# Optimization experiments

Measured on AMD Instinct MI355X. Metric: run time of the kernel, lower is better.

The kernel has to match this reference:

```python
import jax, jax.numpy as jnp
import numpy as np

B, T, K = 256, 512, 128
LR_MULT = 1.0  # learning_rate_multiplier


def setup_inputs() -> dict:
    key = jax.random.key(0)
    k1, k2, k3 = jax.random.split(key, 3)
    emissions = jax.random.normal(k1, (B, T, K), dtype=jnp.float32)
    mask = jax.random.randint(k2, (B, T), 0, 2, dtype=jnp.int32)
    # learned CRF transition matrix (stand-in for Orthogonal init)
    transition_weight = jax.random.normal(k3, (K, K), dtype=jnp.float32)
    return {"emissions": emissions, "mask": mask, "transition_weight": transition_weight}


def reference(emissions, mask, transition_weight):
    # Viterbi decode (tfa.text.crf_decode semantics): sequence_lengths = sum(mask),
    # state frozen for steps t >= length, output tags multiplied by mask.
    mask = mask.astype(jnp.int32)
    lengths = jnp.sum(mask, axis=1)                       # [B]
    trans = transition_weight * LR_MULT                   # [K,K]
    Tn = emissions.shape[1]

    init_state = emissions[:, 0, :]                       # [B,K] viterbi scores at t=0
    ts = jnp.arange(1, Tn)                                # steps 1..T-1
    em_rest = jnp.swapaxes(emissions[:, 1:, :], 0, 1)     # [T-1,B,K]

    def fwd_step(state, inp):
        e_t, t = inp                                      # e_t: [B,K]
        scores = state[:, :, None] + trans[None, :, :]    # [B, K_prev, K_cur]
        bp = jnp.argmax(scores, axis=1).astype(jnp.int32)  # [B,K] best prev tag
        new_state = jnp.max(scores, axis=1) + e_t         # [B,K]
        valid = (t < lengths)[:, None]                    # step valid iff t <= len-1
        return jnp.where(valid, new_state, state), bp

    last_state, bps = jax.lax.scan(fwd_step, init_state, (em_rest, ts))  # bps: [T-1,B,K]
    last_tag = jnp.argmax(last_state, axis=1).astype(jnp.int32)  # tag at pos length-1

    def bwd_step(tag, inp):
        bp_t, t = inp                                     # bp_t: [B,K]
        prev = jnp.take_along_axis(bp_t, tag[:, None], axis=1)[:, 0]
        tag = jnp.where(t < lengths, prev, tag)           # carry tag beyond seq end
        return tag, tag

    # reverse scan: ys[i] = tag at position i, for positions 0..T-2
    _, tags_prefix = jax.lax.scan(bwd_step, last_tag, (bps, ts), reverse=True)
    tags = jnp.concatenate([jnp.swapaxes(tags_prefix, 0, 1), last_tag[:, None]], axis=1)
    return tags * mask
```

## Files before the change

### kernel.cpp

```cpp
#include <hip/hip_runtime.h>

#define NB 256
#define NT 512
#define NK 128

__device__ __forceinline__ void upd(float v, int i, float& bv, int& bi) {
    bool g = v > bv;
    bv = g ? v : bv;
    bi = g ? i : bi;
}

__global__ __launch_bounds__(256, 1)
void crf_decode_kernel(const float* __restrict__ em,
                       const int* __restrict__ mask,
                       const float* __restrict__ trans,
                       int* __restrict__ out) {
    __shared__ alignas(16) float state_sh[NK];
    __shared__ float part_val[256];
    __shared__ int   part_idx[256];
    __shared__ unsigned char bp_sh[(NT - 1) * NK];
    __shared__ int tags_sh[NT];
    __shared__ int len_sh;
    __shared__ int lt_sh;

    const int b    = blockIdx.x;
    const int tid  = threadIdx.x;
    const int j    = tid & (NK - 1);
    const int half = tid >> 7;
    const long base = (long)b * NT * NK;

    int s = mask[b * NT + tid] + mask[b * NT + tid + 256];
    #pragma unroll
    for (int off = 32; off > 0; off >>= 1) s += __shfl_down(s, off, 64);
    if (tid == 0) len_sh = 0;
    __syncthreads();
    if ((tid & 63) == 0) atomicAdd(&len_sh, s);

    if (half == 0) state_sh[j] = em[base + j];

    float treg[64];
    #pragma unroll
    for (int ii = 0; ii < 64; ++ii)
        treg[ii] = trans[(half * 64 + ii) * NK + j];

    __syncthreads();
    const int len = len_sh;

    for (int t = 1; t < len; ++t) {
        float e = 0.0f;
        if (half == 0) e = em[base + t * NK + j];

        float bv0 = -3.4e38f, bv1 = -3.4e38f, bv2 = -3.4e38f, bv3 = -3.4e38f;
        int   bi0 = 0, bi1 = 1, bi2 = 2, bi3 = 3;
        const float4* sp = (const float4*)&state_sh[half * 64];
        #pragma unroll
        for (int g = 0; g < 16; ++g) {
            float4 sv = sp[g];
            const int ib = half * 64 + g * 4;
            upd(sv.x + treg[g * 4 + 0], ib + 0, bv0, bi0);
            upd(sv.y + treg[g * 4 + 1], ib + 1, bv1, bi1);
            upd(sv.z + treg[g * 4 + 2], ib + 2, bv2, bi2);
            upd(sv.w + treg[g * 4 + 3], ib + 3, bv3, bi3);
        }
        bool tk;
        tk = (bv1 > bv0) || (bv1 == bv0 && bi1 < bi0);
        float mv0 = tk ? bv1 : bv0; int mi0 = tk ? bi1 : bi0;
        tk = (bv3 > bv2) || (bv3 == bv2 && bi3 < bi2);
        float mv1 = tk ? bv3 : bv2; int mi1 = tk ? bi3 : bi2;
        tk = (mv1 > mv0) || (mv1 == mv0 && mi1 < mi0);
        float bv = tk ? mv1 : mv0;  int bi = tk ? mi1 : mi0;

        part_val[tid] = bv;
        part_idx[tid] = bi;
        __syncthreads();
        if (half == 0) {
            float ov = part_val[tid + 128];
            int   oi = part_idx[tid + 128];
            bool take = ov > bv;
            float nv = (take ? ov : bv) + e;
            int   ni = take ? oi : bi;
            state_sh[j] = nv;
            bp_sh[(t - 1) * NK + j] = (unsigned char)ni;
        }
        __syncthreads();
    }

    if (tid < 64) {
        float v0 = state_sh[tid], v1 = state_sh[tid + 64];
        bool take = v1 > v0;
        float v = take ? v1 : v0;
        int  ix = take ? tid + 64 : tid;
        #pragma unroll
        for (int off = 32; off > 0; off >>= 1) {
            float vo = __shfl_xor(v, off, 64);
            int   io = __shfl_xor(ix, off, 64);
            bool t2 = (vo > v) || (vo == v && io < ix);
            v  = t2 ? vo : v;
            ix = t2 ? io : ix;
        }
        if (tid == 0) lt_sh = ix;
    }
    __syncthreads();
    const int last_tag = lt_sh;
    const int lm1 = (len > 0) ? (len - 1) : 0;

    for (int p = tid; p < NT; p += 256)
        if (p >= lm1) tags_sh[p] = last_tag;
    __syncthreads();

    if (tid == 0) {
        int tag = last_tag;
        for (int p = lm1 - 1; p >= 0; --p) {
            tag = (int)bp_sh[p * NK + tag];
            tags_sh[p] = tag;
        }
    }
    __syncthreads();

    for (int p = tid; p < NT; p += 256) {
        int mv = mask[b * NT + p];
        out[b * NT + p] = mv ? tags_sh[p] : 0;
    }
}

extern "C" void kernel_launch(void* const* d_in, const int* in_sizes, int n_in,
                              void* d_out, int out_size, void* d_ws, size_t ws_size,
                              hipStream_t stream) {
    const float* em    = (const float*)d_in[0];
    const int*   mask  = (const int*)d_in[1];
    const float* trans = (const float*)d_in[2];
    int* out = (int*)d_out;
    hipLaunchKernelGGL(crf_decode_kernel, dim3(NB), dim3(256), 0, stream,
                       em, mask, trans, out);
}
```

Baseline: 411.2 us.

## Use one thread per tag with double-buffered state and prefetched emissions

Shrinks the block from 256 to 128 threads so each thread reduces over all 128 previous tags itself. This removes the cross-half partial-result exchange, and double-buffering the state array leaves one barrier per time step instead of two. Emissions are prefetched from global memory eight steps ahead into a double-buffered shared array, taking the global load off the per-step critical path. In exchange, each step's serial max/argmax chain is twice as long on fewer waves, and each thread keeps 128 transition values in registers.

```diff
diff --git a/kernel.cpp b/kernel.cpp
--- a/kernel.cpp
+++ b/kernel.cpp
@@ -3,6 +3,7 @@
 #define NB 256
 #define NT 512
 #define NK 128
+#define GRP 8
 
 __device__ __forceinline__ void upd(float v, int i, float& bv, int& bi) {
     bool g = v > bv;
@@ -10,86 +11,86 @@
     bi = g ? i : bi;
 }
 
-__global__ __launch_bounds__(256, 1)
+__global__ __launch_bounds__(128, 1)
 void crf_decode_kernel(const float* __restrict__ em,
                        const int* __restrict__ mask,
                        const float* __restrict__ trans,
                        int* __restrict__ out) {
-    __shared__ alignas(16) float state_sh[NK];
-    __shared__ float part_val[256];
-    __shared__ int   part_idx[256];
+    __shared__ alignas(16) float state_sh[2][NK];
+    __shared__ float e_sh[2][GRP][NK];
     __shared__ unsigned char bp_sh[(NT - 1) * NK];
     __shared__ int tags_sh[NT];
-    __shared__ int len_sh;
-    __shared__ int lt_sh;
+    __shared__ float red_v[2];
+    __shared__ int   red_i[2];
+    __shared__ int len_sh, lt_sh;
 
-    const int b    = blockIdx.x;
-    const int tid  = threadIdx.x;
-    const int j    = tid & (NK - 1);
-    const int half = tid >> 7;
+    const int b = blockIdx.x;
+    const int j = threadIdx.x;
     const long base = (long)b * NT * NK;
 
-    int s = mask[b * NT + tid] + mask[b * NT + tid + 256];
+    float ld[GRP];
+    #pragma unroll
+    for (int k = 0; k < GRP; ++k) ld[k] = em[base + (1 + k) * NK + j];
+
+    int s = 0;
+    #pragma unroll
+    for (int k = 0; k < 4; ++k) s += mask[b * NT + j + 128 * k];
     #pragma unroll
     for (int off = 32; off > 0; off >>= 1) s += __shfl_down(s, off, 64);
-    if (tid == 0) len_sh = 0;
+    if (j == 0) len_sh = 0;
     __syncthreads();
-    if ((tid & 63) == 0) atomicAdd(&len_sh, s);
+    if ((j & 63) == 0) atomicAdd(&len_sh, s);
 
-    if (half == 0) state_sh[j] = em[base + j];
+    float treg[NK];
+    #pragma unroll
+    for (int i = 0; i < NK; ++i) treg[i] = trans[i * NK + j];
 
-    float treg[64];
-    #pragma unroll
-    for (int ii = 0; ii < 64; ++ii)
-        treg[ii] = trans[(half * 64 + ii) * NK + j];
-
+    state_sh[0][j] = em[base + j];
     __syncthreads();
     const int len = len_sh;
 
-    for (int t = 1; t < len; ++t) {
-        float e = 0.0f;
-        if (half == 0) e = em[base + t * NK + j];
+    int cur = 0, cb = 0;
+    for (int t0 = 1; t0 < len; t0 += GRP) {
+        #pragma unroll
+        for (int k = 0; k < GRP; ++k) e_sh[cb][k][j] = ld[k];
+        #pragma unroll
+        for (int k = 0; k < GRP; ++k) {
+            int tt = t0 + GRP + k; tt = tt < NT ? tt : NT - 1;
+            ld[k] = em[base + tt * NK + j];
+        }
+        const int te = (t0 + GRP < len) ? t0 + GRP : len;
+        for (int t = t0; t < te; ++t) {
+            const float4* sp = (const float4*)state_sh[cur];
+            float bv0 = -3.4e38f, bv1 = -3.4e38f, bv2 = -3.4e38f, bv3 = -3.4e38f;
+            int   bi0 = 0, bi1 = 1, bi2 = 2, bi3 = 3;
+            #pragma unroll
+            for (int g = 0; g < 32; ++g) {
+                float4 sv = sp[g];
+                upd(sv.x + treg[4 * g + 0], 4 * g + 0, bv0, bi0);
+                upd(sv.y + treg[4 * g + 1], 4 * g + 1, bv1, bi1);
+                upd(sv.z + treg[4 * g + 2], 4 * g + 2, bv2, bi2);
+                upd(sv.w + treg[4 * g + 3], 4 * g + 3, bv3, bi3);
+            }
+            bool tk;
+            tk = (bv1 > bv0) || (bv1 == bv0 && bi1 < bi0);
+            float mv0 = tk ? bv1 : bv0; int mi0 = tk ? bi1 : bi0;
+            tk = (bv3 > bv2) || (bv3 == bv2 && bi3 < bi2);
+            float mv1 = tk ? bv3 : bv2; int mi1 = tk ? bi3 : bi2;
+            tk = (mv1 > mv0) || (mv1 == mv0 && mi1 < mi0);
+            float bv = tk ? mv1 : mv0;  int bi = tk ? mi1 : mi0;
 
-        float bv0 = -3.4e38f, bv1 = -3.4e38f, bv2 = -3.4e38f, bv3 = -3.4e38f;
-        int   bi0 = 0, bi1 = 1, bi2 = 2, bi3 = 3;
-        const float4* sp = (const float4*)&state_sh[half * 64];
-        #pragma unroll
-        for (int g = 0; g < 16; ++g) {
-            float4 sv = sp[g];
-            const int ib = half * 64 + g * 4;
-            upd(sv.x + treg[g * 4 + 0], ib + 0, bv0, bi0);
-            upd(sv.y + treg[g * 4 + 1], ib + 1, bv1, bi1);
-            upd(sv.z + treg[g * 4 + 2], ib + 2, bv2, bi2);
-            upd(sv.w + treg[g * 4 + 3], ib + 3, bv3, bi3);
+            float e = e_sh[cb][t - t0][j];
+            state_sh[cur ^ 1][j] = bv + e;
+            bp_sh[(t - 1) * NK + j] = (unsigned char)bi;
+            __syncthreads();
+            cur ^= 1;
         }
-        bool tk;
-        tk = (bv1 > bv0) || (bv1 == bv0 && bi1 < bi0);
-        float mv0 = tk ? bv1 : bv0; int mi0 = tk ? bi1 : bi0;
-        tk = (bv3 > bv2) || (bv3 == bv2 && bi3 < bi2);
-        float mv1 = tk ? bv3 : bv2; int mi1 = tk ? bi3 : bi2;
-        tk = (mv1 > mv0) || (mv1 == mv0 && mi1 < mi0);
-        float bv = tk ? mv1 : mv0;  int bi = tk ? mi1 : mi0;
-
-        part_val[tid] = bv;
-        part_idx[tid] = bi;
-        __syncthreads();
-        if (half == 0) {
-            float ov = part_val[tid + 128];
-            int   oi = part_idx[tid + 128];
-            bool take = ov > bv;
-            float nv = (take ? ov : bv) + e;
-            int   ni = take ? oi : bi;
-            state_sh[j] = nv;
-            bp_sh[(t - 1) * NK + j] = (unsigned char)ni;
-        }
-        __syncthreads();
+        cb ^= 1;
     }
 
-    if (tid < 64) {
-        float v0 = state_sh[tid], v1 = state_sh[tid + 64];
-        bool take = v1 > v0;
-        float v = take ? v1 : v0;
-        int  ix = take ? tid + 64 : tid;
+    {
+        float v = state_sh[cur][j];
+        int  ix = j;
         #pragma unroll
         for (int off = 32; off > 0; off >>= 1) {
             float vo = __shfl_xor(v, off, 64);
@@ -98,17 +99,24 @@
             v  = t2 ? vo : v;
             ix = t2 ? io : ix;
         }
-        if (tid == 0) lt_sh = ix;
+        if ((j & 63) == 0) { red_v[j >> 6] = v; red_i[j >> 6] = ix; }
+        __syncthreads();
+        if (j == 0) {
+            float v0 = red_v[0], v1 = red_v[1];
+            int   i0 = red_i[0], i1 = red_i[1];
+            bool t2 = (v1 > v0) || (v1 == v0 && i1 < i0);
+            lt_sh = t2 ? i1 : i0;
+        }
     }
     __syncthreads();
     const int last_tag = lt_sh;
     const int lm1 = (len > 0) ? (len - 1) : 0;
 
-    for (int p = tid; p < NT; p += 256)
+    for (int p = j; p < NT; p += 128)
         if (p >= lm1) tags_sh[p] = last_tag;
     __syncthreads();
 
-    if (tid == 0) {
+    if (j == 0) {
         int tag = last_tag;
         for (int p = lm1 - 1; p >= 0; --p) {
             tag = (int)bp_sh[p * NK + tag];
@@ -117,7 +125,7 @@
     }
     __syncthreads();
 
-    for (int p = tid; p < NT; p += 256) {
+    for (int p = j; p < NT; p += 128) {
         int mv = mask[b * NT + p];
         out[b * NT + p] = mv ? tags_sh[p] : 0;
     }
@@ -130,6 +138,6 @@
     const int*   mask  = (const int*)d_in[1];
     const float* trans = (const float*)d_in[2];
     int* out = (int*)d_out;
-    hipLaunchKernelGGL(crf_decode_kernel, dim3(NB), dim3(256), 0, stream,
+    hipLaunchKernelGGL(crf_decode_kernel, dim3(NB), dim3(128), 0, stream,
                        em, mask, trans, out);
 }
```

New measurement: 679.0 us. 65.1% more time.

## Pair halves within a wavefront, double-buffer state, prefetch emissions in groups

Applied to the files above, without the earlier changes.

Remaps threads so the two halves of each tag's reduction sit in the same wavefront, replacing the shared-memory partial exchange with a cross-lane shuffle. State is double-buffered so each time step needs one barrier instead of two. Emission values are prefetched eight steps ahead into registers to hide global load latency in the serial recurrence. This raises register pressure through the extra prefetch registers, and the tail loop loads emissions without prefetching.

```diff
diff --git a/kernel.cpp b/kernel.cpp
--- a/kernel.cpp
+++ b/kernel.cpp
@@ -3,6 +3,7 @@
 #define NB 256
 #define NT 512
 #define NK 128
+#define GRP 8
 
 __device__ __forceinline__ void upd(float v, int i, float& bv, int& bi) {
     bool g = v > bv;
@@ -15,18 +16,17 @@
                        const int* __restrict__ mask,
                        const float* __restrict__ trans,
                        int* __restrict__ out) {
-    __shared__ alignas(16) float state_sh[NK];
-    __shared__ float part_val[256];
-    __shared__ int   part_idx[256];
+    __shared__ alignas(16) float state_sh[2][NK];
     __shared__ unsigned char bp_sh[(NT - 1) * NK];
     __shared__ int tags_sh[NT];
-    __shared__ int len_sh;
-    __shared__ int lt_sh;
+    __shared__ int len_sh, lt_sh;
 
     const int b    = blockIdx.x;
     const int tid  = threadIdx.x;
-    const int j    = tid & (NK - 1);
-    const int half = tid >> 7;
+    const int l    = tid & 63;
+    const int w    = tid >> 6;
+    const int jj   = (w << 5) | (l & 31);
+    const int half = l >> 5;
     const long base = (long)b * NT * NK;
 
     int s = mask[b * NT + tid] + mask[b * NT + tid + 256];
@@ -34,33 +34,39 @@
     for (int off = 32; off > 0; off >>= 1) s += __shfl_down(s, off, 64);
     if (tid == 0) len_sh = 0;
     __syncthreads();
-    if ((tid & 63) == 0) atomicAdd(&len_sh, s);
-
-    if (half == 0) state_sh[j] = em[base + j];
+    if (l == 0) atomicAdd(&len_sh, s);
 
     float treg[64];
     #pragma unroll
     for (int ii = 0; ii < 64; ++ii)
-        treg[ii] = trans[(half * 64 + ii) * NK + j];
+        treg[ii] = trans[(half * 64 + ii) * NK + jj];
 
+    if (half == 0) state_sh[0][jj] = em[base + jj];
     __syncthreads();
     const int len = len_sh;
 
-    for (int t = 1; t < len; ++t) {
-        float e = 0.0f;
-        if (half == 0) e = em[base + t * NK + j];
+    int cur = 0;
+    int t = 1;
 
+    float ld[GRP];
+    #pragma unroll
+    for (int k = 0; k < GRP; ++k) {
+        int tt = t + k; tt = tt < NT ? tt : NT - 1;
+        ld[k] = em[base + tt * NK + jj];
+    }
+
+    auto step = [&](int tt, float e) {
+        const float4* sp = (const float4*)&state_sh[cur][half * 64];
         float bv0 = -3.4e38f, bv1 = -3.4e38f, bv2 = -3.4e38f, bv3 = -3.4e38f;
-        int   bi0 = 0, bi1 = 1, bi2 = 2, bi3 = 3;
-        const float4* sp = (const float4*)&state_sh[half * 64];
+        int bi0 = half*64 + 0, bi1 = half*64 + 1, bi2 = half*64 + 2, bi3 = half*64 + 3;
         #pragma unroll
         for (int g = 0; g < 16; ++g) {
             float4 sv = sp[g];
-            const int ib = half * 64 + g * 4;
-            upd(sv.x + treg[g * 4 + 0], ib + 0, bv0, bi0);
-            upd(sv.y + treg[g * 4 + 1], ib + 1, bv1, bi1);
-            upd(sv.z + treg[g * 4 + 2], ib + 2, bv2, bi2);
-            upd(sv.w + treg[g * 4 + 3], ib + 3, bv3, bi3);
+            const int ib = half * 64 + 4 * g;
+            upd(sv.x + treg[4*g + 0], ib + 0, bv0, bi0);
+            upd(sv.y + treg[4*g + 1], ib + 1, bv1, bi1);
+            upd(sv.z + treg[4*g + 2], ib + 2, bv2, bi2);
+            upd(sv.w + treg[4*g + 3], ib + 3, bv3, bi3);
         }
         bool tk;
         tk = (bv1 > bv0) || (bv1 == bv0 && bi1 < bi0);
@@ -70,23 +76,38 @@
         tk = (mv1 > mv0) || (mv1 == mv0 && mi1 < mi0);
         float bv = tk ? mv1 : mv0;  int bi = tk ? mi1 : mi0;
 
-        part_val[tid] = bv;
-        part_idx[tid] = bi;
+        float vo = __shfl_xor(bv, 32, 64);
+        int   io = __shfl_xor(bi, 32, 64);
+        bool t2 = (vo > bv) || (vo == bv && io < bi);
+        float fv = t2 ? vo : bv;
+        int   fi = t2 ? io : bi;
+
+        if (half == 0) state_sh[cur ^ 1][jj] = fv + e;
+        else           bp_sh[(tt - 1) * NK + jj] = (unsigned char)fi;
         __syncthreads();
-        if (half == 0) {
-            float ov = part_val[tid + 128];
-            int   oi = part_idx[tid + 128];
-            bool take = ov > bv;
-            float nv = (take ? ov : bv) + e;
-            int   ni = take ? oi : bi;
-            state_sh[j] = nv;
-            bp_sh[(t - 1) * NK + j] = (unsigned char)ni;
+        cur ^= 1;
+    };
+
+    while (t + GRP <= len) {
+        float ec[GRP];
+        #pragma unroll
+        for (int k = 0; k < GRP; ++k) ec[k] = ld[k];
+        #pragma unroll
+        for (int k = 0; k < GRP; ++k) {
+            int tt = t + GRP + k; tt = tt < NT ? tt : NT - 1;
+            ld[k] = em[base + tt * NK + jj];
         }
-        __syncthreads();
+        #pragma unroll
+        for (int k = 0; k < GRP; ++k) step(t + k, ec[k]);
+        t += GRP;
+    }
+    for (; t < len; ++t) {
+        float e = em[base + t * NK + jj];
+        step(t, e);
     }
 
     if (tid < 64) {
-        float v0 = state_sh[tid], v1 = state_sh[tid + 64];
+        float v0 = state_sh[cur][tid], v1 = state_sh[cur][tid + 64];
         bool take = v1 > v0;
         float v = take ? v1 : v0;
         int  ix = take ? tid + 64 : tid;
```

New measurement: 379.0 us. 7.8% less time.
